# Kernel tuning notes

Hardware: AMD Instinct MI355X
Metric: run time of the kernel (lower is better)

Reference implementation:

```python
import jax, jax.numpy as jnp
import numpy as np

NIN, NOUT = 256, 64

def setup_inputs() -> dict:
    key = jax.random.key(0)
    k1, k2, k3, k4 = jax.random.split(key, 4)
    B, T = 4, 4096
    y = jax.random.normal(k1, (B, T, NIN), dtype=jnp.float32)
    # torch Linear(nin, nout).weight has shape [nout, nin]; store as [nin, nout]
    s = 1.0 / np.sqrt(NIN)
    Wq = jax.random.uniform(k2, (NIN, NOUT), jnp.float32, -s, s)
    Wk = jax.random.uniform(k3, (NIN, NOUT), jnp.float32, -s, s)
    Wv = jax.random.uniform(k4, (NIN, NOUT), jnp.float32, -s, s)
    return {"y": y, "Wq": Wq, "Wk": Wk, "Wv": Wv}

def reference(y, Wq, Wk, Wv):
    T = y.shape[1]
    que = y @ Wq  # [B,T,NOUT]
    key = y @ Wk
    val = y @ Wv
    att = jnp.einsum('bqd,bkd->bqk', que, key)  # [B,T,T]
    causal = jnp.tril(jnp.ones((T, T), dtype=bool))  # True = keep
    att = jnp.where(causal, att, -jnp.inf)
    att = jax.nn.softmax(att / jnp.sqrt(jnp.float32(NOUT)), axis=-1)
    return jnp.einsum('bqk,bkd->bqd', att, val)
```

## Files before the change

### kernel.cpp

```cpp
#include <hip/hip_runtime.h>
#include <hip/hip_bf16.h>

#define TLEN 4096
#define NINP 256
#define DD   64

#define QSCALE 0.18033688011112042f

typedef __attribute__((ext_vector_type(8))) short bf16x8;
typedef __attribute__((ext_vector_type(4))) short bf16x4;
typedef __attribute__((ext_vector_type(4))) float f32x4;

union U8 { bf16x8 v; uint u[4]; };
union U4 { bf16x4 v; uint u[2]; };

__device__ inline ushort bfu(float x) {
    union { float f; uint u; } a; a.f = x;
    uint r = a.u + 0x7fffu + ((a.u >> 16) & 1u);
    return (ushort)(r >> 16);
}
__device__ inline uint pk2(float lo, float hi) {
    return (uint)bfu(lo) | ((uint)bfu(hi) << 16);
}
__device__ inline uint cvtpk(float lo, float hi) {
    uint r;
    asm("v_cvt_pk_bf16_f32 %0, %1, %2" : "=v"(r) : "v"(lo), "v"(hi));
    return r;
}

__device__ inline bf16x8 ld16(const ushort* p) {
    return *(const bf16x8*)p;
}

__global__ __launch_bounds__(256) void prep_wt(
    const float* __restrict__ Wq, const float* __restrict__ Wk,
    const float* __restrict__ Wv, ushort* __restrict__ WTf)
{
    __shared__ ushort lt[256 * 66];
    const int t = threadIdx.x;
    const int m = blockIdx.x;
    const float* W = (m == 0) ? Wq : ((m == 1) ? Wk : Wv);
    const float scale = (m == 0) ? QSCALE : 1.0f;

    #pragma unroll
    for (int j = 0; j < 16; ++j) {
        int i4 = t + 256 * j;
        float4 v = *(const float4*)&W[i4 * 4];
        int k = i4 >> 4, d = (i4 * 4) & 63;
        *(uint*)&lt[k * 66 + d]     = pk2(v.x * scale, v.y * scale);
        *(uint*)&lt[k * 66 + d + 2] = pk2(v.z * scale, v.w * scale);
    }
    __syncthreads();
    #pragma unroll
    for (int j = 0; j < 8; ++j) {
        int slot = t + 256 * j;
        int u = slot >> 6, ln = slot & 63;
        int s = u >> 2, nt = u & 3;
        int d = nt * 16 + (ln & 15);
        int k0 = s * 32 + (ln >> 4) * 8;
        uint a0 = (uint)lt[(k0 + 0) * 66 + d] | ((uint)lt[(k0 + 1) * 66 + d] << 16);
        uint a1 = (uint)lt[(k0 + 2) * 66 + d] | ((uint)lt[(k0 + 3) * 66 + d] << 16);
        uint a2 = (uint)lt[(k0 + 4) * 66 + d] | ((uint)lt[(k0 + 5) * 66 + d] << 16);
        uint a3 = (uint)lt[(k0 + 6) * 66 + d] | ((uint)lt[(k0 + 7) * 66 + d] << 16);
        ushort* gd = WTf + m * 16384 + slot * 8;
        ((uint2*)gd)[0] = uint2{a0, a1};
        ((uint2*)gd)[1] = uint2{a2, a3};
    }
}

__global__ __launch_bounds__(768) void qkv_kernel(
    const float* __restrict__ y, const ushort* __restrict__ WTf,
    ushort* __restrict__ Qh, ushort* __restrict__ Kp, ushort* __restrict__ Vp)
{
    __shared__ ushort tb[3][64 * 68];

    const int t = threadIdx.x;
    const int w = t >> 6, lane = t & 63;
    const int quad = lane >> 4, l15 = lane & 15;
    const int mb = w >> 2;
    const int g  = w & 3;
    const int rb = blockIdx.x;
    const int rowbase = rb * 64;
    const int myrow = rowbase + g * 16 + l15;

    bf16x8 afrag[8];
    const float* yrow = y + (size_t)myrow * NINP;
    #pragma unroll
    for (int s = 0; s < 8; ++s) {
        float4 lo = *(const float4*)&yrow[s * 32 + quad * 8];
        float4 hi = *(const float4*)&yrow[s * 32 + quad * 8 + 4];
        U8 u;
        u.u[0] = pk2(lo.x, lo.y);
        u.u[1] = pk2(lo.z, lo.w);
        u.u[2] = pk2(hi.x, hi.y);
        u.u[3] = pk2(hi.z, hi.w);
        afrag[s] = u.v;
    }

    f32x4 acc[4];
    #pragma unroll
    for (int nt = 0; nt < 4; ++nt) acc[nt] = f32x4{0.f, 0.f, 0.f, 0.f};

    const ushort* Wm = WTf + mb * 16384 + lane * 8;
    #pragma unroll
    for (int s = 0; s < 8; ++s)
        #pragma unroll
        for (int nt = 0; nt < 4; ++nt) {
            bf16x8 bfrag = ld16(Wm + (s * 4 + nt) * 512);
            acc[nt] = __builtin_amdgcn_mfma_f32_16x16x32_bf16(
                afrag[s], bfrag, acc[nt], 0, 0, 0);
        }

    if (mb < 2) {
        #pragma unroll
        for (int nt = 0; nt < 4; ++nt)
            #pragma unroll
            for (int r = 0; r < 4; ++r)
                tb[mb][(g * 16 + quad * 4 + r) * 68 + nt * 16 + l15] = bfu(acc[nt][r]);
    } else {
        #pragma unroll
        for (int nt = 0; nt < 4; ++nt) {
            int d = nt * 16 + l15;
            #pragma unroll
            for (int r = 0; r < 4; r += 2) {
                int tt = g * 16 + quad * 4 + r;
                *(uint*)&tb[2][d * 68 + tt] = pk2(acc[nt][r], acc[nt][r + 1]);
            }
        }
    }
    __syncthreads();

    const int tl = t & 255;
    if (mb == 0) {
        int row = tl >> 2, seg = tl & 3;
        ushort* gd = Qh + (size_t)(rowbase + row) * DD + seg * 16;
        const ushort* sp = &tb[0][row * 68 + seg * 16];
        #pragma unroll
        for (int j = 0; j < 4; ++j) ((uint2*)gd)[j] = ((const uint2*)sp)[j];
    } else if (mb == 1) {
        #pragma unroll
        for (int j = 0; j < 2; ++j) {
            int idx = tl + 256 * j;
            int instr = idx >> 6, ln = idx & 63;
            int kt = instr >> 1, s = instr & 1;
            int q2 = ln >> 4, l15b = ln & 15;
            int row = kt * 16 + l15b, dcol = s * 32 + q2 * 8;
            const ushort* sp = &tb[1][row * 68 + dcol];
            ushort* gd = Kp + (size_t)rb * 4096 + idx * 8;
            ((uint2*)gd)[0] = ((const uint2*)sp)[0];
            ((uint2*)gd)[1] = ((const uint2*)sp)[1];
        }
    } else {
        #pragma unroll
        for (int j = 0; j < 2; ++j) {
            int idx = tl + 256 * j;
            int instr = idx >> 6, ln = idx & 63;
            int nt = instr >> 1, m = instr & 1;
            int q2 = ln >> 4, l15b = ln & 15;
            int d = nt * 16 + l15b;
            int k0 = 32 * m + q2 * 4;
            ushort* gd = Vp + (size_t)rb * 4096 + idx * 8;
            ((uint2*)gd)[0] = *(const uint2*)&tb[2][d * 68 + k0];
            ((uint2*)gd)[1] = *(const uint2*)&tb[2][d * 68 + k0 + 16];
        }
    }
}

__device__ inline void load_k32(bf16x8 (&kf)[2][2], const ushort* __restrict__ Kw,
                                int ci)
{
    const ushort* base = Kw + (size_t)ci * 2048;
    #pragma unroll
    for (int kt = 0; kt < 2; ++kt)
        #pragma unroll
        for (int s = 0; s < 2; ++s)
            kf[kt][s] = ld16(base + (kt * 2 + s) * 512);
}

__device__ inline void load_v32(U4 (&vt)[4][2], const ushort* __restrict__ Vw,
                                int ci)
{
    const ushort* base = Vw + (size_t)(ci >> 1) * 4096 + (ci & 1) * 512;
    #pragma unroll
    for (int nt = 0; nt < 4; ++nt) {
        U8 uu; uu.v = ld16(base + nt * 1024);
        vt[nt][0].u[0] = uu.u[0]; vt[nt][0].u[1] = uu.u[1];
        vt[nt][1].u[0] = uu.u[2]; vt[nt][1].u[1] = uu.u[3];
    }
}

__device__ inline void chunk32(
    const bf16x8 (&kf)[2][2], bf16x8 (&kfn)[2][2],
    const ushort* __restrict__ Kw, const ushort* __restrict__ Vw,
    const bf16x8 (&qf)[2][2], f32x4 (&oT)[2][4], float (&l_acc)[2],
    int ci, int pf, int chi, int qb, int quad, int l15)
{
    const int c0 = ci * 32;
    U4 vt[4][2];
    load_v32(vt, Vw, ci);

    f32x4 st[2][2];
    #pragma unroll
    for (int qt = 0; qt < 2; ++qt)
        #pragma unroll
        for (int kt = 0; kt < 2; ++kt)
            st[qt][kt] = f32x4{0.f, 0.f, 0.f, 0.f};
    __builtin_amdgcn_s_setprio(1);
    #pragma unroll
    for (int s = 0; s < 2; ++s)
        #pragma unroll
        for (int qt = 0; qt < 2; ++qt)
            #pragma unroll
            for (int kt = 0; kt < 2; ++kt)
                st[qt][kt] = __builtin_amdgcn_mfma_f32_16x16x32_bf16(
                    kf[kt][s], qf[qt][s], st[qt][kt], 0, 0, 0);
    __builtin_amdgcn_s_setprio(0);

    if (pf < chi) load_k32(kfn, Kw, pf);

    U4 pa[2][2];
    if (c0 + 31 <= qb) {
        #pragma unroll
        for (int qt = 0; qt < 2; ++qt)
            #pragma unroll
            for (int kt = 0; kt < 2; ++kt) {
                float p0 = exp2f(st[qt][kt][0]);
                float p1 = exp2f(st[qt][kt][1]);
                float p2 = exp2f(st[qt][kt][2]);
                float p3 = exp2f(st[qt][kt][3]);
                l_acc[qt] += (p0 + p1) + (p2 + p3);
                pa[qt][kt].u[0] = cvtpk(p0, p1);
                pa[qt][kt].u[1] = cvtpk(p2, p3);
            }
    } else {
        #pragma unroll
        for (int qt = 0; qt < 2; ++qt) {
            const int q = qb + qt * 16 + l15;
            #pragma unroll
            for (int kt = 0; kt < 2; ++kt) {
                const int kb0 = c0 + kt * 16 + quad * 4;
                float p[4];
                #pragma unroll
                for (int r = 0; r < 4; ++r) {
                    float e = exp2f(st[qt][kt][r]);
                    p[r] = (kb0 + r <= q) ? e : 0.f;
                    l_acc[qt] += p[r];
                }
                pa[qt][kt].u[0] = cvtpk(p[0], p[1]);
                pa[qt][kt].u[1] = cvtpk(p[2], p[3]);
            }
        }
    }

    __builtin_amdgcn_s_setprio(1);
    #pragma unroll
    for (int qt = 0; qt < 2; ++qt)
        #pragma unroll
        for (int nt = 0; nt < 4; ++nt)
            #pragma unroll
            for (int kt = 0; kt < 2; ++kt)
                oT[qt][nt] = __builtin_amdgcn_mfma_f32_16x16x16bf16_1k(
                    vt[nt][kt].v, pa[qt][kt].v, oT[qt][nt], 0, 0, 0);
    __builtin_amdgcn_s_setprio(0);
}

__global__ __launch_bounds__(768, 3) void attn_kernel(
    const ushort* __restrict__ Qh, const ushort* __restrict__ Kp,
    const ushort* __restrict__ Vp, float* __restrict__ out)
{
    __shared__ float Ob[12][32 * 68];
    __shared__ float lb[12][32];

    const int t = threadIdx.x;
    const int w = t >> 6, lane = t & 63;
    const int quad = lane >> 4, l15 = lane & 15;

    const int x  = blockIdx.x & 7;
    const int b  = x >> 1;
    const int pr = (((int)blockIdx.x >> 3) << 1) | (x & 1);

    const ushort* Qb = Qh + (size_t)b * TLEN * DD;
    const ushort* Kw = Kp + (size_t)b * 64 * 4096 + lane * 8;
    const ushort* Vw = Vp + (size_t)b * 64 * 4096 + lane * 8;
    float* outb = out + (size_t)b * TLEN * DD;

    for (int half = 0; half < 2; ++half) {
        const int tile = half ? (127 - pr) : pr;
        const int seg  = half ? (11 - w) : w;
        const int qb   = tile * 32;
        const int nc   = tile + 1;
        const int cps  = (nc + 11) / 12;
        const int clo  = seg * cps;
        const int chi  = (nc < clo + cps) ? nc : (clo + cps);

        f32x4 oT[2][4];
        #pragma unroll
        for (int qt = 0; qt < 2; ++qt)
            #pragma unroll
            for (int nt = 0; nt < 4; ++nt)
                oT[qt][nt] = f32x4{0.f, 0.f, 0.f, 0.f};
        float l_acc[2] = {0.f, 0.f};

        if (clo < chi) {
            bf16x8 qf[2][2];
            #pragma unroll
            for (int qt = 0; qt < 2; ++qt)
                #pragma unroll
                for (int s = 0; s < 2; ++s)
                    qf[qt][s] = ld16(Qb + (size_t)(qb + qt * 16 + l15) * DD + s * 32 + quad * 8);

            bf16x8 kfA[2][2], kfB[2][2];
            load_k32(kfA, Kw, clo);
            if (clo + 1 < chi) load_k32(kfB, Kw, clo + 1);

            for (int ci = clo; ci < chi; ci += 2) {
                chunk32(kfA, kfA, Kw, Vw, qf, oT, l_acc,
                        ci, ci + 2, chi, qb, quad, l15);
                if (ci + 1 < chi)
                    chunk32(kfB, kfB, Kw, Vw, qf, oT, l_acc,
                            ci + 1, ci + 3, chi, qb, quad, l15);
            }

            #pragma unroll
            for (int qt = 0; qt < 2; ++qt) {
                l_acc[qt] += __shfl_xor(l_acc[qt], 16, 64);
                l_acc[qt] += __shfl_xor(l_acc[qt], 32, 64);
            }
        }

        #pragma unroll
        for (int qt = 0; qt < 2; ++qt) {
            #pragma unroll
            for (int nt = 0; nt < 4; ++nt)
                #pragma unroll
                for (int r = 0; r < 4; ++r)
                    Ob[w][(qt * 16 + l15) * 68 + nt * 16 + quad * 4 + r] = oT[qt][nt][r];
            if (quad == 0) lb[w][qt * 16 + l15] = l_acc[qt];
        }
        __syncthreads();

        #pragma unroll
        for (int e = 0; e < 3; ++e) {
            int idx = t + 768 * e;
            if (idx < 2048) {
                int q = idx >> 6, d = idx & 63;
                float s = 0.f, ls = 0.f;
                #pragma unroll
                for (int ww = 0; ww < 12; ++ww) {
                    s += Ob[ww][q * 68 + d];
                    ls += lb[ww][q];
                }
                outb[(size_t)(qb + q) * DD + d] = s * __builtin_amdgcn_rcpf(ls);
            }
        }
        __syncthreads();
    }
}

extern "C" void kernel_launch(void* const* d_in, const int* in_sizes, int n_in,
                              void* d_out, int out_size, void* d_ws, size_t ws_size,
                              hipStream_t stream) {
    const float* y  = (const float*)d_in[0];
    const float* Wq = (const float*)d_in[1];
    const float* Wk = (const float*)d_in[2];
    const float* Wv = (const float*)d_in[3];
    float* outp = (float*)d_out;

    const int rows = in_sizes[0] / NINP;
    const int nb = rows / TLEN;
    const int rbn = rows / 64;

    ushort* WT = (ushort*)d_ws;
    ushort* Qh = WT + 3 * 16384;
    ushort* Kp = Qh + (size_t)rows * DD;
    ushort* Vp = Kp + (size_t)rows * DD;

    prep_wt<<<3, 256, 0, stream>>>(Wq, Wk, Wv, WT);
    qkv_kernel<<<rbn, 768, 0, stream>>>(y, WT, Qh, Kp, Vp);
    attn_kernel<<<nb * 64, 768, 0, stream>>>(Qh, Kp, Vp, outp);
}
```

Before: 101.7 us.

## Fuse weight prep, QKV projection and attention into one cooperative kernel

Merges the three launches (weight transpose/convert, QKV projection, causal attention) into a single cooperative kernel with grid-wide syncs between phases, sharing LDS through a union. The goal is to remove two kernel launch gaps and their tail effects. In exchange it adds two grid.sync barriers. It also requires all 256 blocks of 768 threads to be co-resident, which depends on the occupancy allowed by launch bounds and LDS.

```diff
diff --git a/kernel.cpp b/kernel.cpp
--- a/kernel.cpp
+++ b/kernel.cpp
@@ -1,5 +1,8 @@
 #include <hip/hip_runtime.h>
 #include <hip/hip_bf16.h>
+#include <hip/hip_cooperative_groups.h>
+
+namespace cg = cooperative_groups;
 
 #define TLEN 4096
 #define NINP 256
@@ -30,140 +33,6 @@
 
 __device__ inline bf16x8 ld16(const ushort* p) {
     return *(const bf16x8*)p;
-}
-
-__global__ __launch_bounds__(256) void prep_wt(
-    const float* __restrict__ Wq, const float* __restrict__ Wk,
-    const float* __restrict__ Wv, ushort* __restrict__ WTf)
-{
-    __shared__ ushort lt[256 * 66];
-    const int t = threadIdx.x;
-    const int m = blockIdx.x;
-    const float* W = (m == 0) ? Wq : ((m == 1) ? Wk : Wv);
-    const float scale = (m == 0) ? QSCALE : 1.0f;
-
-    #pragma unroll
-    for (int j = 0; j < 16; ++j) {
-        int i4 = t + 256 * j;
-        float4 v = *(const float4*)&W[i4 * 4];
-        int k = i4 >> 4, d = (i4 * 4) & 63;
-        *(uint*)&lt[k * 66 + d]     = pk2(v.x * scale, v.y * scale);
-        *(uint*)&lt[k * 66 + d + 2] = pk2(v.z * scale, v.w * scale);
-    }
-    __syncthreads();
-    #pragma unroll
-    for (int j = 0; j < 8; ++j) {
-        int slot = t + 256 * j;
-        int u = slot >> 6, ln = slot & 63;
-        int s = u >> 2, nt = u & 3;
-        int d = nt * 16 + (ln & 15);
-        int k0 = s * 32 + (ln >> 4) * 8;
-        uint a0 = (uint)lt[(k0 + 0) * 66 + d] | ((uint)lt[(k0 + 1) * 66 + d] << 16);
-        uint a1 = (uint)lt[(k0 + 2) * 66 + d] | ((uint)lt[(k0 + 3) * 66 + d] << 16);
-        uint a2 = (uint)lt[(k0 + 4) * 66 + d] | ((uint)lt[(k0 + 5) * 66 + d] << 16);
-        uint a3 = (uint)lt[(k0 + 6) * 66 + d] | ((uint)lt[(k0 + 7) * 66 + d] << 16);
-        ushort* gd = WTf + m * 16384 + slot * 8;
-        ((uint2*)gd)[0] = uint2{a0, a1};
-        ((uint2*)gd)[1] = uint2{a2, a3};
-    }
-}
-
-__global__ __launch_bounds__(768) void qkv_kernel(
-    const float* __restrict__ y, const ushort* __restrict__ WTf,
-    ushort* __restrict__ Qh, ushort* __restrict__ Kp, ushort* __restrict__ Vp)
-{
-    __shared__ ushort tb[3][64 * 68];
-
-    const int t = threadIdx.x;
-    const int w = t >> 6, lane = t & 63;
-    const int quad = lane >> 4, l15 = lane & 15;
-    const int mb = w >> 2;
-    const int g  = w & 3;
-    const int rb = blockIdx.x;
-    const int rowbase = rb * 64;
-    const int myrow = rowbase + g * 16 + l15;
-
-    bf16x8 afrag[8];
-    const float* yrow = y + (size_t)myrow * NINP;
-    #pragma unroll
-    for (int s = 0; s < 8; ++s) {
-        float4 lo = *(const float4*)&yrow[s * 32 + quad * 8];
-        float4 hi = *(const float4*)&yrow[s * 32 + quad * 8 + 4];
-        U8 u;
-        u.u[0] = pk2(lo.x, lo.y);
-        u.u[1] = pk2(lo.z, lo.w);
-        u.u[2] = pk2(hi.x, hi.y);
-        u.u[3] = pk2(hi.z, hi.w);
-        afrag[s] = u.v;
-    }
-
-    f32x4 acc[4];
-    #pragma unroll
-    for (int nt = 0; nt < 4; ++nt) acc[nt] = f32x4{0.f, 0.f, 0.f, 0.f};
-
-    const ushort* Wm = WTf + mb * 16384 + lane * 8;
-    #pragma unroll
-    for (int s = 0; s < 8; ++s)
-        #pragma unroll
-        for (int nt = 0; nt < 4; ++nt) {
-            bf16x8 bfrag = ld16(Wm + (s * 4 + nt) * 512);
-            acc[nt] = __builtin_amdgcn_mfma_f32_16x16x32_bf16(
-                afrag[s], bfrag, acc[nt], 0, 0, 0);
-        }
-
-    if (mb < 2) {
-        #pragma unroll
-        for (int nt = 0; nt < 4; ++nt)
-            #pragma unroll
-            for (int r = 0; r < 4; ++r)
-                tb[mb][(g * 16 + quad * 4 + r) * 68 + nt * 16 + l15] = bfu(acc[nt][r]);
-    } else {
-        #pragma unroll
-        for (int nt = 0; nt < 4; ++nt) {
-            int d = nt * 16 + l15;
-            #pragma unroll
-            for (int r = 0; r < 4; r += 2) {
-                int tt = g * 16 + quad * 4 + r;
-                *(uint*)&tb[2][d * 68 + tt] = pk2(acc[nt][r], acc[nt][r + 1]);
-            }
-        }
-    }
-    __syncthreads();
-
-    const int tl = t & 255;
-    if (mb == 0) {
-        int row = tl >> 2, seg = tl & 3;
-        ushort* gd = Qh + (size_t)(rowbase + row) * DD + seg * 16;
-        const ushort* sp = &tb[0][row * 68 + seg * 16];
-        #pragma unroll
-        for (int j = 0; j < 4; ++j) ((uint2*)gd)[j] = ((const uint2*)sp)[j];
-    } else if (mb == 1) {
-        #pragma unroll
-        for (int j = 0; j < 2; ++j) {
-            int idx = tl + 256 * j;
-            int instr = idx >> 6, ln = idx & 63;
-            int kt = instr >> 1, s = instr & 1;
-            int q2 = ln >> 4, l15b = ln & 15;
-            int row = kt * 16 + l15b, dcol = s * 32 + q2 * 8;
-            const ushort* sp = &tb[1][row * 68 + dcol];
-            ushort* gd = Kp + (size_t)rb * 4096 + idx * 8;
-            ((uint2*)gd)[0] = ((const uint2*)sp)[0];
-            ((uint2*)gd)[1] = ((const uint2*)sp)[1];
-        }
-    } else {
-        #pragma unroll
-        for (int j = 0; j < 2; ++j) {
-            int idx = tl + 256 * j;
-            int instr = idx >> 6, ln = idx & 63;
-            int nt = instr >> 1, m = instr & 1;
-            int q2 = ln >> 4, l15b = ln & 15;
-            int d = nt * 16 + l15b;
-            int k0 = 32 * m + q2 * 4;
-            ushort* gd = Vp + (size_t)rb * 4096 + idx * 8;
-            ((uint2*)gd)[0] = *(const uint2*)&tb[2][d * 68 + k0];
-            ((uint2*)gd)[1] = *(const uint2*)&tb[2][d * 68 + k0 + 16];
-        }
-    }
 }
 
 __device__ inline void load_k32(bf16x8 (&kf)[2][2], const ushort* __restrict__ Kw,
@@ -264,96 +133,228 @@
     __builtin_amdgcn_s_setprio(0);
 }
 
-__global__ __launch_bounds__(768, 3) void attn_kernel(
-    const ushort* __restrict__ Qh, const ushort* __restrict__ Kp,
-    const ushort* __restrict__ Vp, float* __restrict__ out)
+__global__ __launch_bounds__(768, 3) void fused_kernel(
+    const float* __restrict__ y,
+    const float* __restrict__ Wq, const float* __restrict__ Wk,
+    const float* __restrict__ Wv,
+    ushort* __restrict__ WTf, ushort* __restrict__ Qh,
+    ushort* __restrict__ Kp, ushort* __restrict__ Vp,
+    float* __restrict__ out)
 {
-    __shared__ float Ob[12][32 * 68];
-    __shared__ float lb[12][32];
+    __shared__ union {
+        ushort lt[256 * 66];
+        ushort tb[3][64 * 68];
+        struct { float Ob[12][32 * 68]; float lb[12][32]; } at;
+    } sm;
+
+    cg::grid_group grid = cg::this_grid();
 
     const int t = threadIdx.x;
     const int w = t >> 6, lane = t & 63;
     const int quad = lane >> 4, l15 = lane & 15;
 
-    const int x  = blockIdx.x & 7;
-    const int b  = x >> 1;
-    const int pr = (((int)blockIdx.x >> 3) << 1) | (x & 1);
-
-    const ushort* Qb = Qh + (size_t)b * TLEN * DD;
-    const ushort* Kw = Kp + (size_t)b * 64 * 4096 + lane * 8;
-    const ushort* Vw = Vp + (size_t)b * 64 * 4096 + lane * 8;
-    float* outb = out + (size_t)b * TLEN * DD;
-
-    for (int half = 0; half < 2; ++half) {
-        const int tile = half ? (127 - pr) : pr;
-        const int seg  = half ? (11 - w) : w;
-        const int qb   = tile * 32;
-        const int nc   = tile + 1;
-        const int cps  = (nc + 11) / 12;
-        const int clo  = seg * cps;
-        const int chi  = (nc < clo + cps) ? nc : (clo + cps);
-
-        f32x4 oT[2][4];
-        #pragma unroll
-        for (int qt = 0; qt < 2; ++qt)
+    if (blockIdx.x < 3) {
+        const int m = blockIdx.x;
+        const float* W = (m == 0) ? Wq : ((m == 1) ? Wk : Wv);
+        const float scale = (m == 0) ? QSCALE : 1.0f;
+
+        for (int i4 = t; i4 < 4096; i4 += 768) {
+            float4 v = *(const float4*)&W[i4 * 4];
+            int k = i4 >> 4, d = (i4 * 4) & 63;
+            *(uint*)&sm.lt[k * 66 + d]     = pk2(v.x * scale, v.y * scale);
+            *(uint*)&sm.lt[k * 66 + d + 2] = pk2(v.z * scale, v.w * scale);
+        }
+        __syncthreads();
+        for (int slot = t; slot < 2048; slot += 768) {
+            int u = slot >> 6, ln = slot & 63;
+            int s = u >> 2, nt = u & 3;
+            int d = nt * 16 + (ln & 15);
+            int k0 = s * 32 + (ln >> 4) * 8;
+            uint a0 = (uint)sm.lt[(k0 + 0) * 66 + d] | ((uint)sm.lt[(k0 + 1) * 66 + d] << 16);
+            uint a1 = (uint)sm.lt[(k0 + 2) * 66 + d] | ((uint)sm.lt[(k0 + 3) * 66 + d] << 16);
+            uint a2 = (uint)sm.lt[(k0 + 4) * 66 + d] | ((uint)sm.lt[(k0 + 5) * 66 + d] << 16);
+            uint a3 = (uint)sm.lt[(k0 + 6) * 66 + d] | ((uint)sm.lt[(k0 + 7) * 66 + d] << 16);
+            ushort* gd = WTf + m * 16384 + slot * 8;
+            ((uint2*)gd)[0] = uint2{a0, a1};
+            ((uint2*)gd)[1] = uint2{a2, a3};
+        }
+    }
+    __threadfence();
+    grid.sync();
+
+    {
+        const int mb = w >> 2;
+        const int g  = w & 3;
+        const int rb = blockIdx.x;
+        const int rowbase = rb * 64;
+        const int myrow = rowbase + g * 16 + l15;
+
+        bf16x8 afrag[8];
+        const float* yrow = y + (size_t)myrow * NINP;
+        #pragma unroll
+        for (int s = 0; s < 8; ++s) {
+            float4 lo = *(const float4*)&yrow[s * 32 + quad * 8];
+            float4 hi = *(const float4*)&yrow[s * 32 + quad * 8 + 4];
+            U8 u;
+            u.u[0] = pk2(lo.x, lo.y);
+            u.u[1] = pk2(lo.z, lo.w);
+            u.u[2] = pk2(hi.x, hi.y);
+            u.u[3] = pk2(hi.z, hi.w);
+            afrag[s] = u.v;
+        }
+
+        f32x4 acc[4];
+        #pragma unroll
+        for (int nt = 0; nt < 4; ++nt) acc[nt] = f32x4{0.f, 0.f, 0.f, 0.f};
+
+        const ushort* Wm = WTf + mb * 16384 + lane * 8;
+        #pragma unroll
+        for (int s = 0; s < 8; ++s)
+            #pragma unroll
+            for (int nt = 0; nt < 4; ++nt) {
+                bf16x8 bfrag = ld16(Wm + (s * 4 + nt) * 512);
+                acc[nt] = __builtin_amdgcn_mfma_f32_16x16x32_bf16(
+                    afrag[s], bfrag, acc[nt], 0, 0, 0);
+            }
+
+        if (mb < 2) {
             #pragma unroll
             for (int nt = 0; nt < 4; ++nt)
-                oT[qt][nt] = f32x4{0.f, 0.f, 0.f, 0.f};
-        float l_acc[2] = {0.f, 0.f};
-
-        if (clo < chi) {
-            bf16x8 qf[2][2];
+                #pragma unroll
+                for (int r = 0; r < 4; ++r)
+                    sm.tb[mb][(g * 16 + quad * 4 + r) * 68 + nt * 16 + l15] = bfu(acc[nt][r]);
+        } else {
+            #pragma unroll
+            for (int nt = 0; nt < 4; ++nt) {
+                int d = nt * 16 + l15;
+                #pragma unroll
+                for (int r = 0; r < 4; r += 2) {
+                    int tt = g * 16 + quad * 4 + r;
+                    *(uint*)&sm.tb[2][d * 68 + tt] = pk2(acc[nt][r], acc[nt][r + 1]);
+                }
+            }
+        }
+        __syncthreads();
+
+        const int tl = t & 255;
+        if (mb == 0) {
+            int row = tl >> 2, seg = tl & 3;
+            ushort* gd = Qh + (size_t)(rowbase + row) * DD + seg * 16;
+            const ushort* sp = &sm.tb[0][row * 68 + seg * 16];
+            #pragma unroll
+            for (int j = 0; j < 4; ++j) ((uint2*)gd)[j] = ((const uint2*)sp)[j];
+        } else if (mb == 1) {
+            #pragma unroll
+            for (int j = 0; j < 2; ++j) {
+                int idx = tl + 256 * j;
+                int instr = idx >> 6, ln = idx & 63;
+                int kt = instr >> 1, s = instr & 1;
+                int q2 = ln >> 4, l15b = ln & 15;
+                int row = kt * 16 + l15b, dcol = s * 32 + q2 * 8;
+                const ushort* sp = &sm.tb[1][row * 68 + dcol];
+                ushort* gd = Kp + (size_t)rb * 4096 + idx * 8;
+                ((uint2*)gd)[0] = ((const uint2*)sp)[0];
+                ((uint2*)gd)[1] = ((const uint2*)sp)[1];
+            }
+        } else {
+            #pragma unroll
+            for (int j = 0; j < 2; ++j) {
+                int idx = tl + 256 * j;
+                int instr = idx >> 6, ln = idx & 63;
+                int nt = instr >> 1, m = instr & 1;
+                int q2 = ln >> 4, l15b = ln & 15;
+                int d = nt * 16 + l15b;
+                int k0 = 32 * m + q2 * 4;
+                ushort* gd = Vp + (size_t)rb * 4096 + idx * 8;
+                ((uint2*)gd)[0] = *(const uint2*)&sm.tb[2][d * 68 + k0];
+                ((uint2*)gd)[1] = *(const uint2*)&sm.tb[2][d * 68 + k0 + 16];
+            }
+        }
+    }
+    __threadfence();
+    grid.sync();
+
+    {
+        const int x  = blockIdx.x & 7;
+        const int b  = x >> 1;
+        const int pr = (((int)blockIdx.x >> 3) << 1) | (x & 1);
+
+        const ushort* Qb = Qh + (size_t)b * TLEN * DD;
+        const ushort* Kw = Kp + (size_t)b * 64 * 4096 + lane * 8;
+        const ushort* Vw = Vp + (size_t)b * 64 * 4096 + lane * 8;
+        float* outb = out + (size_t)b * TLEN * DD;
+
+        for (int half = 0; half < 2; ++half) {
+            const int tile = half ? (127 - pr) : pr;
+            const int seg  = half ? (11 - w) : w;
+            const int qb   = tile * 32;
+            const int nc   = tile + 1;
+            const int cps  = (nc + 11) / 12;
+            const int clo  = seg * cps;
+            const int chi  = (nc < clo + cps) ? nc : (clo + cps);
+
+            f32x4 oT[2][4];
             #pragma unroll
             for (int qt = 0; qt < 2; ++qt)
                 #pragma unroll
-                for (int s = 0; s < 2; ++s)
-                    qf[qt][s] = ld16(Qb + (size_t)(qb + qt * 16 + l15) * DD + s * 32 + quad * 8);
-
-            bf16x8 kfA[2][2], kfB[2][2];
-            load_k32(kfA, Kw, clo);
-            if (clo + 1 < chi) load_k32(kfB, Kw, clo + 1);
-
-            for (int ci = clo; ci < chi; ci += 2) {
-                chunk32(kfA, kfA, Kw, Vw, qf, oT, l_acc,
-                        ci, ci + 2, chi, qb, quad, l15);
-                if (ci + 1 < chi)
-                    chunk32(kfB, kfB, Kw, Vw, qf, oT, l_acc,
-                            ci + 1, ci + 3, chi, qb, quad, l15);
+                for (int nt = 0; nt < 4; ++nt)
+                    oT[qt][nt] = f32x4{0.f, 0.f, 0.f, 0.f};
+            float l_acc[2] = {0.f, 0.f};
+
+            if (clo < chi) {
+                bf16x8 qf[2][2];
+                #pragma unroll
+                for (int qt = 0; qt < 2; ++qt)
+                    #pragma unroll
+                    for (int s = 0; s < 2; ++s)
+                        qf[qt][s] = ld16(Qb + (size_t)(qb + qt * 16 + l15) * DD + s * 32 + quad * 8);
+
+                bf16x8 kfA[2][2], kfB[2][2];
+                load_k32(kfA, Kw, clo);
+                if (clo + 1 < chi) load_k32(kfB, Kw, clo + 1);
+
+                for (int ci = clo; ci < chi; ci += 2) {
+                    chunk32(kfA, kfA, Kw, Vw, qf, oT, l_acc,
+                            ci, ci + 2, chi, qb, quad, l15);
+                    if (ci + 1 < chi)
+                        chunk32(kfB, kfB, Kw, Vw, qf, oT, l_acc,
+                                ci + 1, ci + 3, chi, qb, quad, l15);
+                }
+
+                #pragma unroll
+                for (int qt = 0; qt < 2; ++qt) {
+                    l_acc[qt] += __shfl_xor(l_acc[qt], 16, 64);
+                    l_acc[qt] += __shfl_xor(l_acc[qt], 32, 64);
+                }
             }
 
             #pragma unroll
             for (int qt = 0; qt < 2; ++qt) {
-                l_acc[qt] += __shfl_xor(l_acc[qt], 16, 64);
-                l_acc[qt] += __shfl_xor(l_acc[qt], 32, 64);
-            }
-        }
-
-        #pragma unroll
-        for (int qt = 0; qt < 2; ++qt) {
-            #pragma unroll
-            for (int nt = 0; nt < 4; ++nt)
-                #pragma unroll
-                for (int r = 0; r < 4; ++r)
-                    Ob[w][(qt * 16 + l15) * 68 + nt * 16 + quad * 4 + r] = oT[qt][nt][r];
-            if (quad == 0) lb[w][qt * 16 + l15] = l_acc[qt];
-        }
-        __syncthreads();
-
-        #pragma unroll
-        for (int e = 0; e < 3; ++e) {
-            int idx = t + 768 * e;
-            if (idx < 2048) {
-                int q = idx >> 6, d = idx & 63;
-                float s = 0.f, ls = 0.f;
-                #pragma unroll
-                for (int ww = 0; ww < 12; ++ww) {
-                    s += Ob[ww][q * 68 + d];
-                    ls += lb[ww][q];
-                }
-                outb[(size_t)(qb + q) * DD + d] = s * __builtin_amdgcn_rcpf(ls);
-            }
-        }
-        __syncthreads();
+                #pragma unroll
+                for (int nt = 0; nt < 4; ++nt)
+                    #pragma unroll
+                    for (int r = 0; r < 4; ++r)
+                        sm.at.Ob[w][(qt * 16 + l15) * 68 + nt * 16 + quad * 4 + r] = oT[qt][nt][r];
+                if (quad == 0) sm.at.lb[w][qt * 16 + l15] = l_acc[qt];
+            }
+            __syncthreads();
+
+            #pragma unroll
+            for (int e = 0; e < 3; ++e) {
+                int idx = t + 768 * e;
+                if (idx < 2048) {
+                    int q = idx >> 6, d = idx & 63;
+                    float s = 0.f, ls = 0.f;
+                    #pragma unroll
+                    for (int ww = 0; ww < 12; ++ww) {
+                        s += sm.at.Ob[ww][q * 68 + d];
+                        ls += sm.at.lb[ww][q];
+                    }
+                    outb[(size_t)(qb + q) * DD + d] = s * __builtin_amdgcn_rcpf(ls);
+                }
+            }
+            __syncthreads();
+        }
     }
 }
 
@@ -367,7 +368,6 @@
     float* outp = (float*)d_out;
 
     const int rows = in_sizes[0] / NINP;
-    const int nb = rows / TLEN;
     const int rbn = rows / 64;
 
     ushort* WT = (ushort*)d_ws;
@@ -375,7 +375,9 @@
     ushort* Kp = Qh + (size_t)rows * DD;
     ushort* Vp = Kp + (size_t)rows * DD;
 
-    prep_wt<<<3, 256, 0, stream>>>(Wq, Wk, Wv, WT);
-    qkv_kernel<<<rbn, 768, 0, stream>>>(y, WT, Qh, Kp, Vp);
-    attn_kernel<<<nb * 64, 768, 0, stream>>>(Qh, Kp, Vp, outp);
-}
+    void* args[] = { (void*)&y, (void*)&Wq, (void*)&Wk, (void*)&Wv,
+                     (void*)&WT, (void*)&Qh, (void*)&Kp, (void*)&Vp,
+                     (void*)&outp };
+    hipLaunchCooperativeKernel((const void*)fused_kernel,
+                               dim3(rbn), dim3(768), args, 0, stream);
+}
```

Result: slower. 300.7 us (+195.7%).
